# Optimization experiments

Hardware: AMD Instinct MI355X
Metric: run time of the kernel (lower is better)

Reference implementation:

```python
import jax, jax.numpy as jnp
import numpy as np

B, S, HID = 1, 2048, 4096
NH, NKV, HD = 32, 8, 128
EPS = 1e-6
SCALE = HD ** -0.5


def _rope_cos_sin(seq_len, head_dim, base=1000000.0):
    inv_freq = 1.0 / (base ** (np.arange(0, head_dim, 2, dtype=np.float32) / head_dim))
    t = np.arange(seq_len, dtype=np.float32)
    freqs = np.outer(t, inv_freq)                      # [S, HD/2]
    emb = np.concatenate([freqs, freqs], axis=-1)       # [S, HD]
    return jnp.asarray(np.cos(emb))[None], jnp.asarray(np.sin(emb))[None]  # [1,S,HD]


def setup_inputs() -> dict:
    key = jax.random.key(0)
    ks = jax.random.split(key, 8)
    cos, sin = _rope_cos_sin(S, HD)
    inp = {
        "hidden_states": jax.random.normal(ks[0], (B, S, HID), jnp.float32),
        "cos": jnp.broadcast_to(cos, (B, S, HD)),
        "sin": jnp.broadcast_to(sin, (B, S, HD)),
        "Wq": jax.random.normal(ks[1], (NH * HD, HID), jnp.float32) * 0.02,
        "Wk": jax.random.normal(ks[2], (NKV * HD, HID), jnp.float32) * 0.02,
        "Wv": jax.random.normal(ks[3], (NKV * HD, HID), jnp.float32) * 0.02,
        "Wo": jax.random.normal(ks[4], (HID, NH * HD), jnp.float32) * 0.02,
        "q_norm_w": jnp.ones((HD,), jnp.float32),
        "k_norm_w": jnp.ones((HD,), jnp.float32),
    }
    return inp


def _rmsnorm(x, w, eps=EPS):
    var = jnp.mean(jnp.square(x), axis=-1, keepdims=True)
    return x * jax.lax.rsqrt(var + eps) * w


def _rotate_half(x):
    x1, x2 = jnp.split(x, 2, axis=-1)
    return jnp.concatenate([-x2, x1], axis=-1)


def _apply_rope(x, cos, sin):
    # x: [b,s,n,d]; cos/sin: [b,s,d] -> unsqueeze head dim (dim=2)
    c = cos[:, :, None, :]
    s = sin[:, :, None, :]
    return x * c + _rotate_half(x) * s


def reference(hidden_states, cos, sin, Wq, Wk, Wv, Wo, q_norm_w, k_norm_w):
    b, s, _ = hidden_states.shape
    q = (hidden_states @ Wq.T).reshape(b, s, NH, HD)
    k = (hidden_states @ Wk.T).reshape(b, s, NKV, HD)
    v = (hidden_states @ Wv.T).reshape(b, s, NKV, HD)
    # per-head RMSNorm on q and k
    q = _rmsnorm(q, q_norm_w)
    k = _rmsnorm(k, k_norm_w)
    # RoPE
    q = _apply_rope(q, cos, sin)
    k = _apply_rope(k, cos, sin)
    # GQA: expand kv heads to match query heads (group size = NH // NKV)
    g = NH // NKV
    k = jnp.repeat(k, g, axis=2)  # [b,s,NH,d]
    v = jnp.repeat(v, g, axis=2)
    # causal SDPA, layout bsnd
    scores = jnp.einsum("bqhd,bkhd->bhqk", q, k) * SCALE
    causal = jnp.tril(jnp.ones((s, s), dtype=bool))
    scores = jnp.where(causal[None, None], scores, jnp.finfo(scores.dtype).min)
    probs = jax.nn.softmax(scores, axis=-1)
    attn = jnp.einsum("bhqk,bkhd->bqhd", probs, v).reshape(b, s, NH * HD)
    return attn @ Wo.T
```

## Files before the change

kernel.cpp:

```cpp
#include <hip/hip_runtime.h>
#include <hip/hip_bf16.h>
#include <stdint.h>

#define S_LEN 2048
#define HIDD  4096
#define NH    32
#define NKV   8
#define HD    128
#define NQKV  6144
#define ATT_SCALE 0.08838834764831845f
#define LOG2E 1.4426950408889634f

typedef unsigned short u16;
typedef __attribute__((ext_vector_type(8))) short short8;
typedef __attribute__((ext_vector_type(4))) float f32x4;

__device__ __forceinline__ unsigned f2bfbits(float f){
  union{float f; unsigned u;} v; v.f = f;
  return (v.u + 0x7FFFu + ((v.u>>16)&1u)) >> 16;
}
__device__ __forceinline__ float bf2f(u16 b){
  union{unsigned u; float f;} v; v.u = ((unsigned)b)<<16;
  return v.f;
}
__device__ __forceinline__ unsigned packbf(float a, float b){
  return f2bfbits(a) | (f2bfbits(b)<<16);
}
__device__ __forceinline__ unsigned cvtpk(float lo, float hi){
  unsigned r;
  asm("v_cvt_pk_bf16_f32 %0, %1, %2" : "=v"(r) : "v"(lo), "v"(hi));
  return r;
}

#define GLOAD16(g, l) __builtin_amdgcn_global_load_lds( \
    (__attribute__((address_space(1))) void*)(g), \
    (__attribute__((address_space(3))) void*)(l), 16, 0, 0)

#define VMWAIT(n) asm volatile("s_waitcnt vmcnt(" #n ")" ::: "memory")
#define SCHED0() __builtin_amdgcn_sched_barrier(0)

__global__ __launch_bounds__(256) void cvt_all(const float* __restrict__ hs,
                                               const float* __restrict__ Wq,
                                               const float* __restrict__ Wk,
                                               const float* __restrict__ Wv,
                                               u16* __restrict__ Xb,
                                               u16* __restrict__ WQKV){
  const float* src; u16* dst; int n8;
  switch (blockIdx.y){
    case 0: src = hs; dst = Xb;                        n8 = S_LEN*HIDD/8;    break;
    case 1: src = Wq; dst = WQKV;                      n8 = NH*HD*HIDD/8;    break;
    case 2: src = Wk; dst = WQKV + (size_t)NH*HD*HIDD; n8 = NKV*HD*HIDD/8;   break;
    default:src = Wv; dst = WQKV + (size_t)(NH+NKV)*HD*HIDD; n8 = NKV*HD*HIDD/8; break;
  }
  int i = blockIdx.x*256 + threadIdx.x;
  if (i >= n8) return;
  const float4* p = (const float4*)src;
  float4 a = p[2*i], b = p[2*i+1];
  union { unsigned u[4]; short8 s; } o;
  o.u[0] = packbf(a.x, a.y); o.u[1] = packbf(a.z, a.w);
  o.u[2] = packbf(b.x, b.y); o.u[3] = packbf(b.z, b.w);
  *(short8*)(dst + (size_t)i*8) = o.s;
}

__global__ __launch_bounds__(256) void cvt_bf16(const float* __restrict__ in,
                                                u16* __restrict__ out, int n8){
  int i = blockIdx.x*256 + threadIdx.x;
  if (i >= n8) return;
  const float4* p = (const float4*)in;
  float4 a = p[2*i], b = p[2*i+1];
  union { unsigned u[4]; short8 s; } o;
  o.u[0] = packbf(a.x, a.y); o.u[1] = packbf(a.z, a.w);
  o.u[2] = packbf(b.x, b.y); o.u[3] = packbf(b.z, b.w);
  *(short8*)(out + (size_t)i*8) = o.s;
}

template<int BM, int BN, typename OT>
__global__ __launch_bounds__(512) void gemm_4ph(const u16* __restrict__ A,
                                                const u16* __restrict__ B,
                                                OT* __restrict__ C,
                                                int N, int K, int nbx){
  constexpr int MREP = BM/32;
  constexpr int NF   = BN/64;
  constexpr int AH   = BM/128;
  constexpr int ASZ  = BM*64;
  __shared__ __align__(16) char lds[4*ASZ + 65536];

  const int tid = threadIdx.x;
  const int w = tid>>6, lane = tid&63, ln = lane&15, g = lane>>4;
  const int wm = w>>2, wn = w&3;
  const int swz5 = ((ln>>3)&1)<<5;

  const int nwg = gridDim.x, flat = blockIdx.x;
  const int wg = (flat&7)*(nwg>>3) + (flat>>3);
  const int by = wg/nbx, bx = wg - by*nbx;
  const int m0 = by*BM, n0 = bx*BN;

  const int rs   = ((tid>>6)<<4) + ((tid&63)>>2);
  const int ksrc = ((tid&3)<<3) ^ (((tid>>5)&1)<<4);
  const u16* srcA[AH];
  #pragma unroll
  for (int h=0;h<AH;h++) srcA[h] = A + (size_t)(m0 + h*128 + rs)*K + ksrc;
  const u16* srcB[2];
  #pragma unroll
  for (int h=0;h<2;h++)  srcB[h] = B + (size_t)(n0 + h*128 + rs)*K + ksrc;

  #define AREG(bf,kh) (lds + ((bf)*2 + (kh))*ASZ)
  #define BREG(bf,kh) (lds + 4*ASZ + ((bf)*2 + (kh))*16384)

  #define STAGEPT(t, kh, bf) { const int off_ = (t)*64 + (kh)*32;                 \
    _Pragma("unroll") for (int h=0;h<AH;h++)                                      \
      GLOAD16(srcA[h]+off_, AREG(bf,kh) + h*8192 + w*1024);                       \
    _Pragma("unroll") for (int h=0;h<2;h++)                                       \
      GLOAD16(srcB[h]+off_, BREG(bf,kh) + h*8192 + w*1024); }

  f32x4 acc[MREP][NF];
  #pragma unroll
  for (int m=0;m<MREP;m++)
    #pragma unroll
    for (int n=0;n<NF;n++) acc[m][n] = (f32x4){0.f,0.f,0.f,0.f};
  short8 a0_[MREP], b0_[NF], a1_[MREP], b1_[NF];

  #define READ_SET(aset, bset, bf, kh) {                                          \
    _Pragma("unroll") for (int n=0;n<NF;n++)                                      \
      bset[n] = *(const short8*)(BREG(bf,kh) + (wn*NF+n)*1024 + ln*64 + ((g*16)^swz5)); \
    _Pragma("unroll") for (int m=0;m<MREP;m++)                                    \
      aset[m] = *(const short8*)(AREG(bf,kh) + (wm*MREP+m)*1024 + ln*64 + ((g*16)^swz5)); }
  #define MFMA_SET(aset, bset) { __builtin_amdgcn_s_setprio(1);                   \
    _Pragma("unroll") for (int m=0;m<MREP;m++)                                    \
      _Pragma("unroll") for (int n=0;n<NF;n++)                                    \
        acc[m][n] = __builtin_amdgcn_mfma_f32_16x16x32_bf16(aset[m], bset[n], acc[m][n], 0,0,0); \
    __builtin_amdgcn_s_setprio(0); }
  #define BARR() __builtin_amdgcn_s_barrier()
  #define VMST() do{ if constexpr (AH==2) { VMWAIT(4); } else { VMWAIT(3); } }while(0)

  STAGEPT(0,0,0); STAGEPT(0,1,0); STAGEPT(1,0,1);
  VMWAIT(0); BARR(); SCHED0();
  READ_SET(a0_, b0_, 0, 0);

  const int NIT = K>>7;
  #pragma unroll 1
  for (int it=0; it<NIT; ++it){
    const bool last = (it == NIT-1);
    const int t0 = 2*it;
    READ_SET(a1_, b1_, 0, 1);
    STAGEPT(t0+1, 1, 1);
    MFMA_SET(a0_, b0_);
    SCHED0(); VMST(); BARR(); SCHED0();
    READ_SET(a0_, b0_, 1, 0);
    if (!last) STAGEPT(t0+2, 0, 0);
    MFMA_SET(a1_, b1_);
    SCHED0(); if (last) { VMWAIT(0); } else { VMST(); } BARR(); SCHED0();
    READ_SET(a1_, b1_, 1, 1);
    if (!last) STAGEPT(t0+2, 1, 0);
    MFMA_SET(a0_, b0_);
    SCHED0(); if (!last) { VMST(); } BARR(); SCHED0();
    if (!last){ READ_SET(a0_, b0_, 0, 0); STAGEPT(t0+3, 0, 1); }
    MFMA_SET(a1_, b1_);
    if (!last){ SCHED0(); VMST(); BARR(); SCHED0(); }
  }

  #pragma unroll
  for (int mi=0; mi<MREP; mi++)
    #pragma unroll
    for (int n=0; n<NF; n++)
      #pragma unroll
      for (int r=0;r<4;r++){
        int row = m0 + (wm*MREP+mi)*16 + g*4 + r;
        int col = n0 + wn*(NF*16) + n*16 + ln;
        if constexpr (__is_same(OT, u16))
          C[(size_t)row*N + col] = (u16)f2bfbits(acc[mi][n][r]);
        else
          C[(size_t)row*N + col] = acc[mi][n][r];
      }
  #undef AREG
  #undef BREG
  #undef STAGEPT
  #undef READ_SET
  #undef MFMA_SET
  #undef BARR
  #undef VMST
}

__global__ __launch_bounds__(256) void norm_rope(const u16* __restrict__ QKVb,
                                                 const float* __restrict__ cosb,
                                                 const float* __restrict__ sinb,
                                                 const float* __restrict__ qw,
                                                 const float* __restrict__ kw,
                                                 u16* __restrict__ Qn,
                                                 u16* __restrict__ Kn,
                                                 u16* __restrict__ Vt){
  int w = threadIdx.x>>6, lane = threadIdx.x&63;
  int row = blockIdx.x*4 + w;
  int s = row / 48, slot = row - s*48;
  const u16* src = QKVb + (size_t)s*NQKV + slot*HD;
  float x0 = bf2f(src[lane]), x1 = bf2f(src[lane+64]);
  if (slot < 40){
    float ss = x0*x0 + x1*x1;
    #pragma unroll
    for (int off=1; off<64; off<<=1) ss += __shfl_xor(ss, off, 64);
    float r = rsqrtf(ss*(1.0f/128.0f) + 1e-6f);
    const float* wgt = (slot < 32) ? qw : kw;
    float y0 = x0*r*wgt[lane], y1 = x1*r*wgt[lane+64];
    float c0 = cosb[(size_t)s*HD+lane], c1 = cosb[(size_t)s*HD+lane+64];
    float s0 = sinb[(size_t)s*HD+lane], s1 = sinb[(size_t)s*HD+lane+64];
    float o0 = y0*c0 - y1*s0;
    float o1 = y1*c1 + y0*s1;
    float sc = (slot < 32) ? (ATT_SCALE*LOG2E) : 1.0f;
    u16* dst = (slot < 32) ? (Qn + ((size_t)slot*S_LEN + s)*HD)
                           : (Kn + ((size_t)(slot-32)*S_LEN + s)*HD);
    dst[lane]    = (u16)f2bfbits(o0*sc);
    dst[lane+64] = (u16)f2bfbits(o1*sc);
  } else {
    int kvh = slot - 40;
    u16* dst = Vt + (size_t)kvh*HD*S_LEN + s;
    dst[(size_t)lane*S_LEN]      = (u16)f2bfbits(x0);
    dst[(size_t)(lane+64)*S_LEN] = (u16)f2bfbits(x1);
  }
}

__global__ __launch_bounds__(256) void flash_attn(const u16* __restrict__ Qn,
                                                  const u16* __restrict__ Kn,
                                                  const u16* __restrict__ Vt,
                                                  u16* __restrict__ O){
  __shared__ u16 Ks[2][64*128];
  __shared__ u16 Vs[2][128*64];

  const int h = blockIdx.y;
  const int w = threadIdx.x>>6, lane = threadIdx.x&63, ln = lane&15, g = lane>>4;
  const int kvh = h>>2;
  const u16* Qh = Qn + (size_t)h*S_LEN*HD;
  const u16* Kh = Kn + (size_t)kvh*S_LEN*HD;
  const u16* Vh = Vt + (size_t)kvh*HD*S_LEN;

  const int krow_w = w*4 + g;
  const int ksw    = ((krow_w)&7)<<4;
  const int kcol   = ((ln*16) ^ ksw) >> 1;
  const int vrow_w = w*8 + (lane>>3);
  const int vsw    = ((lane>>3)&7)<<4;
  const int vcol   = (((lane&7)*16) ^ vsw) >> 1;

  #define STAGE_K(bufi, t) { \
    int kv0_ = (t)*64; \
    _Pragma("unroll") \
    for (int p=0;p<4;p++){ \
      const u16* ga = Kh + (size_t)(kv0_ + p*16 + krow_w)*HD + kcol; \
      GLOAD16(ga, (char*)&Ks[bufi][0] + p*4096 + w*1024); \
    } \
  }
  #define STAGE_V(bufi, t) { \
    int kv0_ = (t)*64; \
    _Pragma("unroll") \
    for (int p=0;p<4;p++){ \
      const u16* gv = Vh + (size_t)(p*32 + vrow_w)*S_LEN + kv0_ + vcol; \
      GLOAD16(gv, (char*)&Vs[bufi][0] + p*4096 + w*1024); \
    } \
  }

  #pragma unroll 1
  for (int ph=0; ph<2; ph++){
    const int qb = ph ? (31 - blockIdx.x) : blockIdx.x;
    const int q0 = qb*64;
    const int qrow = q0 + w*16 + ln;

    short8 qf[4];
    #pragma unroll
    for (int c=0;c<4;c++)
      qf[c] = *(const short8*)(Qh + (size_t)qrow*HD + c*32 + g*8);

    f32x4 ot[8];
    #pragma unroll
    for (int dt=0;dt<8;dt++) ot[dt] = (f32x4){0.f,0.f,0.f,0.f};
    float m_run = -1e30f, l_run = 0.f;

    const int nt = qb + 1;

    STAGE_K(0, 0); STAGE_V(0, 0);
    __syncthreads();

    for (int t=0; t<nt; ++t){
      const int cur = t&1;
      if (t+1 < nt) STAGE_K(cur^1, t+1);
      const int kv0 = t*64;

      f32x4 st[4];
      #pragma unroll
      for (int mt=0; mt<4; mt++){
        short8 kf[4];
        #pragma unroll
        for (int c=0;c<4;c++)
          kf[c] = *(const short8*)((const char*)&Ks[cur][0]
                      + (mt*16+ln)*256 + ((c*64 + g*16) ^ ((ln&7)<<4)));
        f32x4 acc = (f32x4){0.f,0.f,0.f,0.f};
        __builtin_amdgcn_s_setprio(1);
        #pragma unroll
        for (int c=0;c<4;c++)
          acc = __builtin_amdgcn_mfma_f32_16x16x32_bf16(kf[c], qf[c], acc, 0,0,0);
        __builtin_amdgcn_s_setprio(0);
        st[mt] = acc;
      }

      if (t+1 < nt) STAGE_V(cur^1, t+1);

      float p[4][4];
      float mtile = -1e30f;
      if (t < qb){
        #pragma unroll
        for (int mt=0; mt<4; mt++)
          #pragma unroll
          for (int r=0;r<4;r++){
            p[mt][r] = st[mt][r];
            mtile = fmaxf(mtile, st[mt][r]);
          }
      } else {
        #pragma unroll
        for (int mt=0; mt<4; mt++)
          #pragma unroll
          for (int r=0;r<4;r++){
            int kv = kv0 + mt*16 + 4*g + r;
            float sv = (kv <= qrow) ? st[mt][r] : -1e30f;
            p[mt][r] = sv;
            mtile = fmaxf(mtile, sv);
          }
      }
      mtile = fmaxf(mtile, __shfl_xor(mtile, 16, 64));
      mtile = fmaxf(mtile, __shfl_xor(mtile, 32, 64));

      bool defer = __all(mtile <= m_run + 11.5416f);
      float m_new = defer ? m_run : fmaxf(m_run, mtile);

      float l_tile = 0.f;
      #pragma unroll
      for (int mt=0; mt<4; mt++)
        #pragma unroll
        for (int r=0;r<4;r++){
          float e = exp2f(p[mt][r] - m_new);
          p[mt][r] = e;
          l_tile += e;
        }
      l_tile += __shfl_xor(l_tile, 16, 64);
      l_tile += __shfl_xor(l_tile, 32, 64);
      if (defer){
        l_run += l_tile;
      } else {
        float alpha = exp2f(m_run - m_new);
        l_run = l_run*alpha + l_tile;
        m_run = m_new;
        #pragma unroll
        for (int dt=0;dt<8;dt++) ot[dt] *= alpha;
      }

      short8 pf[2];
      #pragma unroll
      for (int ks2=0; ks2<2; ks2++){
        unsigned pk00 = cvtpk(p[2*ks2  ][0], p[2*ks2  ][1]);
        unsigned pk01 = cvtpk(p[2*ks2  ][2], p[2*ks2  ][3]);
        unsigned pk10 = cvtpk(p[2*ks2+1][0], p[2*ks2+1][1]);
        unsigned pk11 = cvtpk(p[2*ks2+1][2], p[2*ks2+1][3]);
        int src0 = (((2*g  )&3)<<4) | ln;
        int src1 = (((2*g+1)&3)<<4) | ln;
        unsigned t00 = (unsigned)__shfl((int)pk00, src0, 64);
        unsigned t10 = (unsigned)__shfl((int)pk10, src0, 64);
        unsigned t01 = (unsigned)__shfl((int)pk01, src0, 64);
        unsigned t11 = (unsigned)__shfl((int)pk11, src0, 64);
        unsigned u00 = (unsigned)__shfl((int)pk00, src1, 64);
        unsigned u10 = (unsigned)__shfl((int)pk10, src1, 64);
        unsigned u01 = (unsigned)__shfl((int)pk01, src1, 64);
        unsigned u11 = (unsigned)__shfl((int)pk11, src1, 64);
        bool hiv = (g >= 2);
        union { unsigned u[4]; short8 s; } pw;
        pw.u[0] = hiv ? t10 : t00;
        pw.u[1] = hiv ? t11 : t01;
        pw.u[2] = hiv ? u10 : u00;
        pw.u[3] = hiv ? u11 : u01;
        pf[ks2] = pw.s;
      }

      #pragma unroll
      for (int dt=0;dt<8;dt++){
        short8 vf[2];
        #pragma unroll
        for (int ks2=0; ks2<2; ks2++)
          vf[ks2] = *(const short8*)((const char*)&Vs[cur][0]
                      + (dt*16+ln)*128 + ((ks2*64 + g*16) ^ ((ln&7)<<4)));
        __builtin_amdgcn_s_setprio(1);
        #pragma unroll
        for (int ks2=0; ks2<2; ks2++)
          ot[dt] = __builtin_amdgcn_mfma_f32_16x16x32_bf16(vf[ks2], pf[ks2], ot[dt], 0,0,0);
        __builtin_amdgcn_s_setprio(0);
      }
      __syncthreads();
    }

    float inv = 1.0f / l_run;
    u16* orow = O + (size_t)qrow*(NH*HD) + h*HD;
    #pragma unroll
    for (int dt=0;dt<8;dt++){
      #pragma unroll
      for (int rr=0; rr<4; rr+=2){
        unsigned pkd = cvtpk(ot[dt][rr]*inv, ot[dt][rr+1]*inv);
        *(unsigned*)(orow + dt*16 + g*4 + rr) = pkd;
      }
    }
  }
  #undef STAGE_K
  #undef STAGE_V
}

extern "C" void kernel_launch(void* const* d_in, const int* in_sizes, int n_in,
                              void* d_out, int out_size, void* d_ws, size_t ws_size,
                              hipStream_t stream){
  (void)in_sizes; (void)n_in; (void)out_size; (void)ws_size;
  const float* hs   = (const float*)d_in[0];
  const float* cosb = (const float*)d_in[1];
  const float* sinb = (const float*)d_in[2];
  const float* Wq   = (const float*)d_in[3];
  const float* Wk   = (const float*)d_in[4];
  const float* Wv   = (const float*)d_in[5];
  const float* Wo   = (const float*)d_in[6];
  const float* qw   = (const float*)d_in[7];
  const float* kw   = (const float*)d_in[8];
  float* out = (float*)d_out;

  char* ws = (char*)d_ws;
  u16*   Xb    = (u16*)  (ws);
  u16*   WQKV  = (u16*)  (ws + 16777216);
  u16*   QKVb  = (u16*)  (ws + 67108864);
  u16*   attnB = (u16*)  (ws + 94371840);
  u16*   Qn    = (u16*)  (ws + 117440512);
  u16*   Kn    = (u16*)  (ws + 134217728);
  u16*   Vt    = (u16*)  (ws + 138412032);
  u16*   Wob   = WQKV;

  cvt_all<<<dim3(8192, 4), 256, 0, stream>>>(hs, Wq, Wk, Wv, Xb, WQKV);
  gemm_4ph<256,192,u16><<<256, 512, 0, stream>>>(Xb, WQKV, QKVb, NQKV, HIDD, NQKV/192);
  norm_rope<<<(S_LEN*48)/4, 256, 0, stream>>>(QKVb, cosb, sinb, qw, kw, Qn, Kn, Vt);
  cvt_bf16<<<(HIDD*NH*HD/8)/256, 256, 0, stream>>>(Wo, Wob, HIDD*NH*HD/8);
  flash_attn<<<dim3(16, NH), 256, 0, stream>>>(Qn, Kn, Vt, attnB);
  gemm_4ph<128,256,float><<<256, 512, 0, stream>>>(attnB, Wob, out, HIDD, HIDD, HIDD/256);
}
```

Before: 329.6 us.

## Software-pipeline QK^T of next KV tile ahead of current softmax

```diff
diff --git a/kernel.cpp b/kernel.cpp
--- a/kernel.cpp
+++ b/kernel.cpp
@@ -255,6 +255,102 @@
       GLOAD16(gv, (char*)&Vs[bufi][0] + p*4096 + w*1024); \
     } \
   }
+  #define QKT(dst, buf) { \
+    _Pragma("unroll") for (int mt=0; mt<4; mt++){ \
+      short8 kf[4]; \
+      _Pragma("unroll") for (int c=0;c<4;c++) \
+        kf[c] = *(const short8*)((const char*)&Ks[buf][0] \
+                    + (mt*16+ln)*256 + ((c*64 + g*16) ^ ((ln&7)<<4))); \
+      f32x4 qacc = (f32x4){0.f,0.f,0.f,0.f}; \
+      __builtin_amdgcn_s_setprio(1); \
+      _Pragma("unroll") for (int c=0;c<4;c++) \
+        qacc = __builtin_amdgcn_mfma_f32_16x16x32_bf16(kf[c], qf[c], qacc, 0,0,0); \
+      __builtin_amdgcn_s_setprio(0); \
+      dst[mt] = qacc; \
+    } }
+
+  #define TILE_BODY(i, SC, SN) { \
+    VMWAIT(0); \
+    __builtin_amdgcn_s_barrier(); \
+    if ((i)+1 < nt){ \
+      QKT(SN, ((i)+1)&1); \
+      if ((i)+2 < nt) STAGE_K(((i)+2)&1, (i)+2); \
+      STAGE_V(((i)+1)&1, (i)+1); \
+    } \
+    const int kv0 = (i)*64; \
+    float p[4][4]; \
+    float mtile = -1e30f; \
+    if ((i) < qb){ \
+      _Pragma("unroll") for (int mt=0; mt<4; mt++) \
+        _Pragma("unroll") for (int r=0;r<4;r++){ \
+          p[mt][r] = SC[mt][r]; \
+          mtile = fmaxf(mtile, SC[mt][r]); \
+        } \
+    } else { \
+      _Pragma("unroll") for (int mt=0; mt<4; mt++) \
+        _Pragma("unroll") for (int r=0;r<4;r++){ \
+          int kv = kv0 + mt*16 + 4*g + r; \
+          float sv = (kv <= qrow) ? SC[mt][r] : -1e30f; \
+          p[mt][r] = sv; \
+          mtile = fmaxf(mtile, sv); \
+        } \
+    } \
+    mtile = fmaxf(mtile, __shfl_xor(mtile, 16, 64)); \
+    mtile = fmaxf(mtile, __shfl_xor(mtile, 32, 64)); \
+    bool defer = __all(mtile <= m_run + 11.5416f); \
+    float m_new = defer ? m_run : fmaxf(m_run, mtile); \
+    float l_tile = 0.f; \
+    _Pragma("unroll") for (int mt=0; mt<4; mt++) \
+      _Pragma("unroll") for (int r=0;r<4;r++){ \
+        float e = exp2f(p[mt][r] - m_new); \
+        p[mt][r] = e; \
+        l_tile += e; \
+      } \
+    l_tile += __shfl_xor(l_tile, 16, 64); \
+    l_tile += __shfl_xor(l_tile, 32, 64); \
+    if (defer){ \
+      l_run += l_tile; \
+    } else { \
+      float alpha = exp2f(m_run - m_new); \
+      l_run = l_run*alpha + l_tile; \
+      m_run = m_new; \
+      _Pragma("unroll") for (int dt=0;dt<8;dt++) ot[dt] *= alpha; \
+    } \
+    short8 pf[2]; \
+    _Pragma("unroll") for (int ks2=0; ks2<2; ks2++){ \
+      unsigned pk00 = cvtpk(p[2*ks2  ][0], p[2*ks2  ][1]); \
+      unsigned pk01 = cvtpk(p[2*ks2  ][2], p[2*ks2  ][3]); \
+      unsigned pk10 = cvtpk(p[2*ks2+1][0], p[2*ks2+1][1]); \
+      unsigned pk11 = cvtpk(p[2*ks2+1][2], p[2*ks2+1][3]); \
+      int src0 = (((2*g  )&3)<<4) | ln; \
+      int src1 = (((2*g+1)&3)<<4) | ln; \
+      unsigned t00 = (unsigned)__shfl((int)pk00, src0, 64); \
+      unsigned t10 = (unsigned)__shfl((int)pk10, src0, 64); \
+      unsigned t01 = (unsigned)__shfl((int)pk01, src0, 64); \
+      unsigned t11 = (unsigned)__shfl((int)pk11, src0, 64); \
+      unsigned u00 = (unsigned)__shfl((int)pk00, src1, 64); \
+      unsigned u10 = (unsigned)__shfl((int)pk10, src1, 64); \
+      unsigned u01 = (unsigned)__shfl((int)pk01, src1, 64); \
+      unsigned u11 = (unsigned)__shfl((int)pk11, src1, 64); \
+      bool hiv = (g >= 2); \
+      union { unsigned u[4]; short8 s; } pw; \
+      pw.u[0] = hiv ? t10 : t00; \
+      pw.u[1] = hiv ? t11 : t01; \
+      pw.u[2] = hiv ? u10 : u00; \
+      pw.u[3] = hiv ? u11 : u01; \
+      pf[ks2] = pw.s; \
+    } \
+    _Pragma("unroll") for (int dt=0;dt<8;dt++){ \
+      short8 vf[2]; \
+      _Pragma("unroll") for (int ks2=0; ks2<2; ks2++) \
+        vf[ks2] = *(const short8*)((const char*)&Vs[(i)&1][0] \
+                    + (dt*16+ln)*128 + ((ks2*64 + g*16) ^ ((ln&7)<<4))); \
+      __builtin_amdgcn_s_setprio(1); \
+      _Pragma("unroll") for (int ks2=0; ks2<2; ks2++) \
+        ot[dt] = __builtin_amdgcn_mfma_f32_16x16x32_bf16(vf[ks2], pf[ks2], ot[dt], 0,0,0); \
+      __builtin_amdgcn_s_setprio(0); \
+    } \
+  }
 
   #pragma unroll 1
   for (int ph=0; ph<2; ph++){
@@ -275,121 +371,19 @@
     const int nt = qb + 1;
 
     STAGE_K(0, 0); STAGE_V(0, 0);
+    if (nt > 1) STAGE_K(1, 1);
+    VMWAIT(0);
+    __builtin_amdgcn_s_barrier();
+
+    f32x4 stA[4], stB[4];
+    QKT(stA, 0);
+
+    #pragma unroll 1
+    for (int i=0; i<nt; i+=2){
+      TILE_BODY(i, stA, stB);
+      if (i+1 < nt) TILE_BODY(i+1, stB, stA);
+    }
     __syncthreads();
-
-    for (int t=0; t<nt; ++t){
-      const int cur = t&1;
-      if (t+1 < nt) STAGE_K(cur^1, t+1);
-      const int kv0 = t*64;
-
-      f32x4 st[4];
-      #pragma unroll
-      for (int mt=0; mt<4; mt++){
-        short8 kf[4];
-        #pragma unroll
-        for (int c=0;c<4;c++)
-          kf[c] = *(const short8*)((const char*)&Ks[cur][0]
-                      + (mt*16+ln)*256 + ((c*64 + g*16) ^ ((ln&7)<<4)));
-        f32x4 acc = (f32x4){0.f,0.f,0.f,0.f};
-        __builtin_amdgcn_s_setprio(1);
-        #pragma unroll
-        for (int c=0;c<4;c++)
-          acc = __builtin_amdgcn_mfma_f32_16x16x32_bf16(kf[c], qf[c], acc, 0,0,0);
-        __builtin_amdgcn_s_setprio(0);
-        st[mt] = acc;
-      }
-
-      if (t+1 < nt) STAGE_V(cur^1, t+1);
-
-      float p[4][4];
-      float mtile = -1e30f;
-      if (t < qb){
-        #pragma unroll
-        for (int mt=0; mt<4; mt++)
-          #pragma unroll
-          for (int r=0;r<4;r++){
-            p[mt][r] = st[mt][r];
-            mtile = fmaxf(mtile, st[mt][r]);
-          }
-      } else {
-        #pragma unroll
-        for (int mt=0; mt<4; mt++)
-          #pragma unroll
-          for (int r=0;r<4;r++){
-            int kv = kv0 + mt*16 + 4*g + r;
-            float sv = (kv <= qrow) ? st[mt][r] : -1e30f;
-            p[mt][r] = sv;
-            mtile = fmaxf(mtile, sv);
-          }
-      }
-      mtile = fmaxf(mtile, __shfl_xor(mtile, 16, 64));
-      mtile = fmaxf(mtile, __shfl_xor(mtile, 32, 64));
-
-      bool defer = __all(mtile <= m_run + 11.5416f);
-      float m_new = defer ? m_run : fmaxf(m_run, mtile);
-
-      float l_tile = 0.f;
-      #pragma unroll
-      for (int mt=0; mt<4; mt++)
-        #pragma unroll
-        for (int r=0;r<4;r++){
-          float e = exp2f(p[mt][r] - m_new);
-          p[mt][r] = e;
-          l_tile += e;
-        }
-      l_tile += __shfl_xor(l_tile, 16, 64);
-      l_tile += __shfl_xor(l_tile, 32, 64);
-      if (defer){
-        l_run += l_tile;
-      } else {
-        float alpha = exp2f(m_run - m_new);
-        l_run = l_run*alpha + l_tile;
-        m_run = m_new;
-        #pragma unroll
-        for (int dt=0;dt<8;dt++) ot[dt] *= alpha;
-      }
-
-      short8 pf[2];
-      #pragma unroll
-      for (int ks2=0; ks2<2; ks2++){
-        unsigned pk00 = cvtpk(p[2*ks2  ][0], p[2*ks2  ][1]);
-        unsigned pk01 = cvtpk(p[2*ks2  ][2], p[2*ks2  ][3]);
-        unsigned pk10 = cvtpk(p[2*ks2+1][0], p[2*ks2+1][1]);
-        unsigned pk11 = cvtpk(p[2*ks2+1][2], p[2*ks2+1][3]);
-        int src0 = (((2*g  )&3)<<4) | ln;
-        int src1 = (((2*g+1)&3)<<4) | ln;
-        unsigned t00 = (unsigned)__shfl((int)pk00, src0, 64);
-        unsigned t10 = (unsigned)__shfl((int)pk10, src0, 64);
-        unsigned t01 = (unsigned)__shfl((int)pk01, src0, 64);
-        unsigned t11 = (unsigned)__shfl((int)pk11, src0, 64);
-        unsigned u00 = (unsigned)__shfl((int)pk00, src1, 64);
-        unsigned u10 = (unsigned)__shfl((int)pk10, src1, 64);
-        unsigned u01 = (unsigned)__shfl((int)pk01, src1, 64);
-        unsigned u11 = (unsigned)__shfl((int)pk11, src1, 64);
-        bool hiv = (g >= 2);
-        union { unsigned u[4]; short8 s; } pw;
-        pw.u[0] = hiv ? t10 : t00;
-        pw.u[1] = hiv ? t11 : t01;
-        pw.u[2] = hiv ? u10 : u00;
-        pw.u[3] = hiv ? u11 : u01;
-        pf[ks2] = pw.s;
-      }
-
-      #pragma unroll
-      for (int dt=0;dt<8;dt++){
-        short8 vf[2];
-        #pragma unroll
-        for (int ks2=0; ks2<2; ks2++)
-          vf[ks2] = *(const short8*)((const char*)&Vs[cur][0]
-                      + (dt*16+ln)*128 + ((ks2*64 + g*16) ^ ((ln&7)<<4)));
-        __builtin_amdgcn_s_setprio(1);
-        #pragma unroll
-        for (int ks2=0; ks2<2; ks2++)
-          ot[dt] = __builtin_amdgcn_mfma_f32_16x16x32_bf16(vf[ks2], pf[ks2], ot[dt], 0,0,0);
-        __builtin_amdgcn_s_setprio(0);
-      }
-      __syncthreads();
-    }
 
     float inv = 1.0f / l_run;
     u16* orow = O + (size_t)qrow*(NH*HD) + h*HD;
@@ -404,6 +398,8 @@
   }
   #undef STAGE_K
   #undef STAGE_V
+  #undef QKT
+  #undef TILE_BODY
 }
 
 extern "C" void kernel_launch(void* const* d_in, const int* in_sizes, int n_in,
```

Measured after the change: 330.7 us. About the same (+0.3%).
